# Optimization experiments

Measured on AMD Instinct MI355X. Metric: run time of the kernel, lower is better.

The kernel has to match this reference:

```python
import jax, jax.numpy as jnp
import numpy as np

N_HEADS = 16
DIM = 1024
BS, SLEN = 2, 2048
EPS = 1e-12  # F.normalize eps


def setup_inputs() -> dict:
    key = jax.random.key(0)
    ks = jax.random.split(key, 10)
    d = DIM
    inp = {
        "x": jax.random.normal(ks[0], (BS, SLEN, d), dtype=jnp.float32),
        # causal attention mask, as produced by get_masks(causal=True)
        "mask": jnp.tril(jnp.ones((SLEN, SLEN), dtype=bool))[None].repeat(BS, axis=0),
        "Wq": jax.random.normal(ks[1], (d, d), dtype=jnp.float32) / np.sqrt(d),
        "bq": jax.random.normal(ks[2], (d,), dtype=jnp.float32) * 0.02,
        "Wk": jax.random.normal(ks[3], (d, d), dtype=jnp.float32) / np.sqrt(d),
        "bk": jax.random.normal(ks[4], (d,), dtype=jnp.float32) * 0.02,
        "Wv": jax.random.normal(ks[5], (d, d), dtype=jnp.float32) / np.sqrt(d),
        "bv": jax.random.normal(ks[6], (d,), dtype=jnp.float32) * 0.02,
        "Wo": jax.random.normal(ks[7], (d, d), dtype=jnp.float32) / np.sqrt(d),
        "bo": jax.random.normal(ks[8], (d,), dtype=jnp.float32) * 0.02,
        # learnable scale for normalized (cosine) attention
        "attention_scale": jnp.ones((1,), dtype=jnp.float32) / np.sqrt(d // N_HEADS),
    }
    return inp


def _shape(t, bs, h, dph):
    # (bs, len, dim) -> (bs, h, len, dph)
    return t.reshape(bs, -1, h, dph).transpose(0, 2, 1, 3)


def reference(x, mask, Wq, bq, Wk, bk, Wv, bv, Wo, bo, attention_scale):
    bs, qlen, dim = x.shape
    h = N_HEADS
    dph = dim // h

    q = _shape(x @ Wq + bq, bs, h, dph)  # (bs, h, qlen, dph)
    k = _shape(x @ Wk + bk, bs, h, dph)
    v = _shape(x @ Wv + bv, bs, h, dph)

    # normalized (cosine) attention: L2-normalize q and k, learned scale
    q = q / jnp.maximum(jnp.linalg.norm(q, axis=-1, keepdims=True), EPS)
    k = k / jnp.maximum(jnp.linalg.norm(k, axis=-1, keepdims=True), EPS)
    q = q * attention_scale

    scores = jnp.einsum("bhqd,bhkd->bhqk", q, k)  # (bs, h, qlen, klen)
    scores = jnp.where(mask[:, None, :, :], scores, -jnp.inf)
    weights = jax.nn.softmax(scores, axis=-1)

    ctx = jnp.einsum("bhqk,bhkd->bhqd", weights, v)
    ctx = ctx.transpose(0, 2, 1, 3).reshape(bs, qlen, dim)
    return ctx @ Wo + bo
```

## Files before the change

### kernel.cpp

```cpp
#include <hip/hip_runtime.h>
#include <math.h>

#define NH 16
#define DPH 64
#define SLEN 2048
#define BSZ 2
#define DIM 1024
#define NTOK (BSZ * SLEN)
#define LOG2E 1.44269504088896f

typedef unsigned short ushortT;
typedef __attribute__((ext_vector_type(8))) short short8;
typedef __attribute__((ext_vector_type(4))) short s16x4;
typedef __attribute__((ext_vector_type(4))) float f32x4;

typedef __attribute__((address_space(1))) const unsigned int gu32c;
typedef __attribute__((address_space(3))) unsigned int lu32;

__device__ __forceinline__ void gld16(const void* g, void* l) {
    __builtin_amdgcn_global_load_lds((gu32c*)g, (lu32*)l, 16, 0, 0);
}

__device__ __forceinline__ ushortT f2bf(float f) {
    unsigned int u = __builtin_bit_cast(unsigned int, f);
    u = u + 0x7fffu + ((u >> 16) & 1u);
    return (ushortT)(u >> 16);
}

__device__ __forceinline__ unsigned int cvtpk_bf16(float a, float b) {
    unsigned int r;
    asm("v_cvt_pk_bf16_f32 %0, %1, %2" : "=v"(r) : "v"(a), "v"(b));
    return r;
}

__global__ __launch_bounds__(256) void cvt_all(const float* __restrict__ x,
                                               ushortT* __restrict__ xb,
                                               const float* __restrict__ W0, const float* __restrict__ W1,
                                               const float* __restrict__ W2, const float* __restrict__ W3,
                                               ushortT* __restrict__ T0, ushortT* __restrict__ T1,
                                               ushortT* __restrict__ T2, ushortT* __restrict__ T3) {
    __shared__ float tile[64][65];
    const int tid = threadIdx.x;
    const int bid = blockIdx.x;
    if (bid < 2048) {
        size_t i = (size_t)bid * 256 + tid;
        float4 a = *(const float4*)&x[i * 8];
        float4 b = *(const float4*)&x[i * 8 + 4];
        short8 v;
        v[0] = (short)f2bf(a.x); v[1] = (short)f2bf(a.y);
        v[2] = (short)f2bf(a.z); v[3] = (short)f2bf(a.w);
        v[4] = (short)f2bf(b.x); v[5] = (short)f2bf(b.y);
        v[6] = (short)f2bf(b.z); v[7] = (short)f2bf(b.w);
        *(short8*)&xb[i * 8] = v;
        return;
    }
    const int widx = bid - 2048;
    const int z = widx >> 8, rem = widx & 255;
    const float* W = z == 0 ? W0 : z == 1 ? W1 : z == 2 ? W2 : W3;
    ushortT* T = z == 0 ? T0 : z == 1 ? T1 : z == 2 ? T2 : T3;
    const int kb = (rem >> 4) * 64, nb = (rem & 15) * 64;
#pragma unroll
    for (int it = 0; it < 4; it++) {
        int chunk = it * 256 + tid;
        int r = chunk >> 4, c4 = (chunk & 15) * 4;
        *(float4*)&tile[r][c4] = *(const float4*)&W[(size_t)(kb + r) * DIM + nb + c4];
    }
    __syncthreads();
#pragma unroll
    for (int it = 0; it < 2; it++) {
        int chunk = it * 256 + tid;
        int n = chunk >> 3, k8 = (chunk & 7) * 8;
        short8 o;
#pragma unroll
        for (int j = 0; j < 8; j++) o[j] = (short)f2bf(tile[k8 + j][n]);
        *(short8*)&T[(size_t)(nb + n) * DIM + kb + k8] = o;
    }
}

__global__ __launch_bounds__(512, 2) void gemm_qkv8(const ushortT* __restrict__ A,
                                                    const ushortT* __restrict__ Bt,
                                                    const float* __restrict__ bq,
                                                    const float* __restrict__ bk,
                                                    const float* __restrict__ bv,
                                                    const float* __restrict__ ascale,
                                                    ushortT* __restrict__ Qb,
                                                    ushortT* __restrict__ Kb,
                                                    ushortT* __restrict__ VF) {
    __shared__ __align__(16) ushortT lds[65536];
    const int tid = threadIdx.x;
    const int lane = tid & 63, wid = tid >> 6;
    const int wm = wid >> 2, wn = wid & 3;
    const int lo = lane & 15, hi = lane >> 4;
    const int bid = blockIdx.x;
    const int swz = (bid & 7) * 24 + (bid >> 3);
    const int bx = swz % 12, by = swz / 12;
    const int row0 = by * 256, col0 = bx * 256;
    const int srow2 = tid >> 2, sc = tid & 3;
    f32x4 acc[8][4] = {};
    short8 af[4], bfr[4];

    auto stage = [&](int isA, int buf, int ksh, int kt) {
        const ushortT* g = isA ? A : Bt;
        int r0 = isA ? row0 : col0;
        int base = (isA ? 0 : 32768) + (buf * 2 + ksh) * 8192;
#pragma unroll
        for (int r = 0; r < 2; r++) {
            int rl = r * 128 + srow2;
            int gch = sc ^ ((rl >> 1) & 3);
            gld16(&g[(size_t)(r0 + rl) * DIM + kt * 64 + ksh * 32 + gch * 8],
                  &lds[base + r * 4096 + tid * 8]);
        }
    };
    auto loadA = [&](int buf, int ks, int mh) {
        int base = (buf * 2 + ks) * 8192;
#pragma unroll
        for (int mm = 0; mm < 4; mm++) {
            int row = wm * 128 + (mh * 4 + mm) * 16 + lo;
            af[mm] = *(const short8*)&lds[base + row * 32 + (hi ^ ((row >> 1) & 3)) * 8];
        }
    };
    auto loadB = [&](int buf, int ks) {
        int base = 32768 + (buf * 2 + ks) * 8192;
#pragma unroll
        for (int n = 0; n < 4; n++) {
            int row = wn * 64 + n * 16 + lo;
            bfr[n] = *(const short8*)&lds[base + row * 32 + (hi ^ ((row >> 1) & 3)) * 8];
        }
    };
    auto mfma16 = [&](int mh) {
        __builtin_amdgcn_s_setprio(1);
#pragma unroll
        for (int mm = 0; mm < 4; mm++)
#pragma unroll
            for (int n = 0; n < 4; n++)
                acc[mh * 4 + mm][n] = __builtin_amdgcn_mfma_f32_16x16x32_bf16(
                    af[mm], bfr[n], acc[mh * 4 + mm][n], 0, 0, 0);
        __builtin_amdgcn_s_setprio(0);
    };

    stage(1, 0, 0, 0); stage(0, 0, 0, 0);
    stage(1, 0, 1, 0); stage(0, 0, 1, 0);
    stage(1, 1, 0, 1); stage(0, 1, 0, 1);

#pragma unroll 1
    for (int it = 0; it < 8; ++it) {
        const int o = it * 2 + 1;
        const bool more = (it < 7);
        asm volatile("s_waitcnt vmcnt(8)" ::: "memory");
        asm volatile("s_barrier" ::: "memory");
        loadA(0, 0, 0); loadB(0, 0);
        stage(1, 1, 1, o);
        mfma16(0);
        asm volatile("s_barrier" ::: "memory");
        loadA(0, 0, 1);
        stage(0, 1, 1, o);
        mfma16(1);
        asm volatile("s_waitcnt vmcnt(8)" ::: "memory");
        asm volatile("s_barrier" ::: "memory");
        loadA(0, 1, 0); loadB(0, 1);
        if (more) stage(1, 0, 0, o + 1);
        mfma16(0);
        asm volatile("s_barrier" ::: "memory");
        loadA(0, 1, 1);
        if (more) stage(0, 0, 0, o + 1);
        mfma16(1);
        if (more) { asm volatile("s_waitcnt vmcnt(8)" ::: "memory"); }
        else      { asm volatile("s_waitcnt vmcnt(4)" ::: "memory"); }
        asm volatile("s_barrier" ::: "memory");
        loadA(1, 0, 0); loadB(1, 0);
        if (more) stage(1, 0, 1, o + 1);
        mfma16(0);
        asm volatile("s_barrier" ::: "memory");
        loadA(1, 0, 1);
        if (more) stage(0, 0, 1, o + 1);
        mfma16(1);
        if (more) { asm volatile("s_waitcnt vmcnt(8)" ::: "memory"); }
        else      { asm volatile("s_waitcnt vmcnt(0)" ::: "memory"); }
        asm volatile("s_barrier" ::: "memory");
        loadA(1, 1, 0); loadB(1, 1);
        if (more) stage(1, 1, 0, o + 2);
        mfma16(0);
        asm volatile("s_barrier" ::: "memory");
        loadA(1, 1, 1);
        if (more) stage(0, 1, 0, o + 2);
        mfma16(1);
    }
    __syncthreads();

    const int cg = col0 + wn * 64;
    const int which = cg >> 10;
    const int cwin = cg & 1023;
    const int h = cwin >> 6;
    const int t0g = row0 + wm * 128;
    const int b = t0g >> 11, tok0 = t0g & (SLEN - 1);
    const float* bias = which == 0 ? bq : which == 1 ? bk : bv;

    float bb4[4];
#pragma unroll
    for (int n = 0; n < 4; n++) bb4[n] = bias[cwin + n * 16 + lo];
#pragma unroll
    for (int m = 0; m < 8; m++)
#pragma unroll
        for (int n = 0; n < 4; n++)
#pragma unroll
            for (int r = 0; r < 4; r++) acc[m][n][r] += bb4[n];

    if (which < 2) {
        float asc = (which == 0) ? ascale[0] * LOG2E : 1.0f;
#pragma unroll
        for (int m = 0; m < 8; m++)
#pragma unroll
            for (int r = 0; r < 4; r++) {
                float ss = acc[m][0][r] * acc[m][0][r] + acc[m][1][r] * acc[m][1][r] +
                           acc[m][2][r] * acc[m][2][r] + acc[m][3][r] * acc[m][3][r];
#pragma unroll
                for (int o = 8; o > 0; o >>= 1) ss += __shfl_xor(ss, o);
                float sc2 = asc / fmaxf(sqrtf(ss), 1e-12f);
#pragma unroll
                for (int n = 0; n < 4; n++) acc[m][n][r] *= sc2;
            }
    }

    ushortT* tl = &lds[wid * 8192];
    if (which < 2) {
#pragma unroll
        for (int m = 0; m < 8; m++)
#pragma unroll
            for (int n = 0; n < 4; n++)
#pragma unroll
                for (int r = 0; r < 4; r++) {
                    int row = m * 16 + 4 * hi + r;
                    int c = n * 2 + (lo >> 3);
                    tl[row * 64 + ((c ^ (row & 7)) << 3) + (lo & 7)] = f2bf(acc[m][n][r]);
                }
        ushortT* op = which == 0 ? Qb : Kb;
        const size_t base = ((size_t)(b * NH + h) * SLEN + tok0) * DPH;
#pragma unroll
        for (int j = 0; j < 16; j++) {
            int cid = j * 64 + lane;
            int rowL = cid >> 3, c = cid & 7;
            uint4 v = *(const uint4*)&tl[rowL * 64 + ((c ^ (rowL & 7)) << 3)];
            *(uint4*)&op[base + (size_t)cid * 8] = v;
        }
    } else {
#pragma unroll
        for (int m = 0; m < 8; m++)
#pragma unroll
            for (int n = 0; n < 4; n++)
#pragma unroll
                for (int r = 0; r < 4; r++) {
                    int row = m * 16 + 4 * hi + r;
                    int c = n * 2 + (lo >> 3);
                    tl[row * 64 + ((c ^ ((row >> 3) & 7)) << 3) + (lo & 7)] = f2bf(acc[m][n][r]);
                }
        const int bh = b * NH + h;
        const int kt0 = tok0 >> 6;
#pragma unroll
        for (int i = 0; i < 16; i++) {
            int kk = i >> 3;
            int c = i & 7;
            int jd = c >> 1, ks2 = c & 1;
            int colL = jd * 16 + lo;
            int c2 = colL >> 3;
            short8 v;
#pragma unroll
            for (int e = 0; e < 8; e++) {
                int rowL = kk * 64 + ks2 * 32 + 8 * hi + e;
                v[e] = (short)tl[rowL * 64 + ((c2 ^ ((rowL >> 3) & 7)) << 3) + (colL & 7)];
            }
            *(short8*)&VF[((size_t)bh * 32 + kt0 + kk) * 4096 + (size_t)(c * 64 + lane) * 8] = v;
        }
    }
}

__global__ __launch_bounds__(512, 2) void gemm_oproj(const ushortT* __restrict__ A,
                                                     const ushortT* __restrict__ Bt,
                                                     const float* __restrict__ bias,
                                                     float* __restrict__ outF) {
    __shared__ __align__(16) ushortT lds[32768];
    const int tid = threadIdx.x;
    const int lane = tid & 63, wid = tid >> 6;
    const int wm = wid >> 2, wn = wid & 3;
    const int lo = lane & 15, hi = lane >> 4;
    const int bid = blockIdx.x;
    const int swz = (bid & 7) * 32 + (bid >> 3);
    const int bx = swz & 7, by = swz >> 3;
    const int row0 = by * 128, col0 = bx * 128;
    const int srow = tid >> 2, sc = tid & 3;
    f32x4 acc[4][2] = {};
    short8 afO[2], bfO[2];

    auto stage = [&](int isA, int buf, int ksh, int kt) {
        const ushortT* g = isA ? A : Bt;
        int r0 = isA ? row0 : col0;
        int base = (isA ? 0 : 16384) + (buf * 2 + ksh) * 4096;
        int gch = sc ^ ((srow >> 1) & 3);
        gld16(&g[(size_t)(r0 + srow) * DIM + kt * 64 + ksh * 32 + gch * 8],
              &lds[base + tid * 8]);
    };
    auto loadAO = [&](int buf, int ks, int mh) {
        int base = (buf * 2 + ks) * 4096;
#pragma unroll
        for (int mm = 0; mm < 2; mm++) {
            int row = wm * 64 + (mh * 2 + mm) * 16 + lo;
            afO[mm] = *(const short8*)&lds[base + row * 32 + (hi ^ ((row >> 1) & 3)) * 8];
        }
    };
    auto loadBO = [&](int buf, int ks) {
        int base = 16384 + (buf * 2 + ks) * 4096;
#pragma unroll
        for (int n = 0; n < 2; n++) {
            int row = wn * 32 + n * 16 + lo;
            bfO[n] = *(const short8*)&lds[base + row * 32 + (hi ^ ((row >> 1) & 3)) * 8];
        }
    };
    auto mfma4 = [&](int mh) {
        __builtin_amdgcn_s_setprio(1);
#pragma unroll
        for (int mm = 0; mm < 2; mm++)
#pragma unroll
            for (int n = 0; n < 2; n++)
                acc[mh * 2 + mm][n] = __builtin_amdgcn_mfma_f32_16x16x32_bf16(
                    afO[mm], bfO[n], acc[mh * 2 + mm][n], 0, 0, 0);
        __builtin_amdgcn_s_setprio(0);
    };

    stage(1, 0, 0, 0); stage(0, 0, 0, 0);
    stage(1, 0, 1, 0); stage(0, 0, 1, 0);
    stage(1, 1, 0, 1); stage(0, 1, 0, 1);

#pragma unroll 1
    for (int it = 0; it < 8; ++it) {
        const int o = it * 2 + 1;
        const bool more = (it < 7);
        asm volatile("s_waitcnt vmcnt(4)" ::: "memory");
        asm volatile("s_barrier" ::: "memory");
        loadAO(0, 0, 0); loadBO(0, 0);
        stage(1, 1, 1, o);
        mfma4(0);
        asm volatile("s_barrier" ::: "memory");
        loadAO(0, 0, 1);
        stage(0, 1, 1, o);
        mfma4(1);
        asm volatile("s_waitcnt vmcnt(4)" ::: "memory");
        asm volatile("s_barrier" ::: "memory");
        loadAO(0, 1, 0); loadBO(0, 1);
        if (more) stage(1, 0, 0, o + 1);
        mfma4(0);
        asm volatile("s_barrier" ::: "memory");
        loadAO(0, 1, 1);
        if (more) stage(0, 0, 0, o + 1);
        mfma4(1);
        if (more) { asm volatile("s_waitcnt vmcnt(4)" ::: "memory"); }
        else      { asm volatile("s_waitcnt vmcnt(2)" ::: "memory"); }
        asm volatile("s_barrier" ::: "memory");
        loadAO(1, 0, 0); loadBO(1, 0);
        if (more) stage(1, 0, 1, o + 1);
        mfma4(0);
        asm volatile("s_barrier" ::: "memory");
        loadAO(1, 0, 1);
        if (more) stage(0, 0, 1, o + 1);
        mfma4(1);
        if (more) { asm volatile("s_waitcnt vmcnt(4)" ::: "memory"); }
        else      { asm volatile("s_waitcnt vmcnt(0)" ::: "memory"); }
        asm volatile("s_barrier" ::: "memory");
        loadAO(1, 1, 0); loadBO(1, 1);
        if (more) stage(1, 1, 0, o + 2);
        mfma4(0);
        asm volatile("s_barrier" ::: "memory");
        loadAO(1, 1, 1);
        if (more) stage(0, 1, 0, o + 2);
        mfma4(1);
    }
    __syncthreads();

    float bb[2];
#pragma unroll
    for (int n = 0; n < 2; n++) bb[n] = bias[col0 + wn * 32 + n * 16 + lo];
#pragma unroll
    for (int m = 0; m < 4; m++)
#pragma unroll
        for (int n = 0; n < 2; n++)
#pragma unroll
            for (int r = 0; r < 4; r++) acc[m][n][r] += bb[n];

    float* tl = (float*)&lds[wid * 4096];
#pragma unroll
    for (int m = 0; m < 4; m++)
#pragma unroll
        for (int n = 0; n < 2; n++)
#pragma unroll
            for (int r = 0; r < 4; r++) {
                int row = m * 16 + hi * 4 + r;
                int col = n * 16 + lo;
                int cc = col >> 2;
                tl[row * 32 + ((cc ^ (row & 7)) << 2) + (col & 3)] = acc[m][n][r];
            }
#pragma unroll
    for (int j = 0; j < 8; j++) {
        int cid = j * 64 + lane;
        int rowR = cid >> 3, cc = cid & 7;
        f32x4 v = *(const f32x4*)&tl[rowR * 32 + ((cc ^ (rowR & 7)) << 2)];
        int rg = row0 + wm * 64 + rowR;
        int cgl = col0 + wn * 32 + cc * 4;
        *(f32x4*)&outF[(size_t)rg * DIM + cgl] = v;
    }
}

__global__ __launch_bounds__(512, 4) void attn(const ushortT* __restrict__ Q,
                                               const ushortT* __restrict__ K,
                                               const ushortT* __restrict__ VF,
                                               const float* __restrict__ scale,
                                               ushortT* __restrict__ ctx) {
    __shared__ __align__(16) ushortT Ks[2][64 * 64];
    __shared__ __align__(16) ushortT Ps[8 * 16 * 64];
    const int tid = threadIdx.x, lane = tid & 63, wid = tid >> 6;
    const int wg = wid & 3, sg = wid >> 2;
    const int bh = blockIdx.x, p = blockIdx.y;
    const int qt = sg ? p : 31 - p;
    const int kbmax = 31 - p;
    const size_t hb = (size_t)bh * SLEN * DPH;
    const int lo = lane & 15, hi = lane >> 4;
    const float mshift = fabsf(scale[0]) * LOG2E;

    short8 aq[2];
    {
        const int qrow = qt * 64 + wg * 16 + lo;
#pragma unroll
        for (int ks = 0; ks < 2; ks++)
            aq[ks] = *(const short8*)&Q[hb + (size_t)qrow * DPH + ks * 32 + 8 * hi];
    }

    const int srow = tid >> 3, sslot = tid & 7;
    const int sldsoff = srow * 64 + ((sslot ^ (srow & 7)) << 3);
    uint4 kr = *(const uint4*)&K[hb + (size_t)srow * DPH + sslot * 8];
    *(uint4*)&Ks[0][sldsoff] = kr;
    __syncthreads();

    f32x4 accd[4] = {};
    float lp = 0.f;

    for (int kb = 0; kb <= kbmax; kb++) {
        const int cur = kb & 1;
        if (kb < kbmax)
            kr = *(const uint4*)&K[hb + (size_t)((kb + 1) * 64 + srow) * DPH + sslot * 8];

        if (kb <= qt) {
            short8 bv[8];
            const ushortT* vt = &VF[(((size_t)bh * 32 + kb) * 512 + lane) * 8];
#pragma unroll
            for (int c = 0; c < 8; c++) bv[c] = *(const short8*)&vt[(size_t)c * 512];

            f32x4 sf[4] = {};
            __builtin_amdgcn_s_setprio(1);
#pragma unroll
            for (int ks = 0; ks < 2; ks++)
#pragma unroll
                for (int j = 0; j < 4; j++) {
                    int row = j * 16 + lo;
                    short8 bk = *(const short8*)&Ks[cur][row * 64 + (((ks * 4 + hi) ^ (row & 7)) << 3)];
                    sf[j] = __builtin_amdgcn_mfma_f32_16x16x32_bf16(bk, aq[ks], sf[j], 0, 0, 0);
                }
            __builtin_amdgcn_s_setprio(0);

            if (kb == qt) {
#pragma unroll
                for (int j = 0; j < 4; j++)
#pragma unroll
                    for (int r = 0; r < 4; r++)
                        if (j * 16 + 4 * hi + r > wg * 16 + lo) sf[j][r] = -INFINITY;
            }

#pragma unroll
            for (int j = 0; j < 4; j++) {
                float pv0 = __builtin_amdgcn_exp2f(sf[j][0] - mshift);
                float pv1 = __builtin_amdgcn_exp2f(sf[j][1] - mshift);
                float pv2 = __builtin_amdgcn_exp2f(sf[j][2] - mshift);
                float pv3 = __builtin_amdgcn_exp2f(sf[j][3] - mshift);
                lp += (pv0 + pv1) + (pv2 + pv3);
                uint2 pk;
                pk.x = cvtpk_bf16(pv0, pv1);
                pk.y = cvtpk_bf16(pv2, pv3);
                int slot = (4 * j + hi) ^ (2 * (lo & 7));
                *(uint2*)&Ps[wid * 1024 + lo * 64 + slot * 4] = pk;
            }

            __builtin_amdgcn_s_setprio(1);
#pragma unroll
            for (int ks = 0; ks < 2; ks++) {
                int slot0 = (8 * ks + 2 * hi) ^ (2 * (lo & 7));
                short8 ap = *(const short8*)&Ps[wid * 1024 + lo * 64 + slot0 * 4];
#pragma unroll
                for (int jd = 0; jd < 4; jd++)
                    accd[jd] = __builtin_amdgcn_mfma_f32_16x16x32_bf16(ap, bv[jd * 2 + ks], accd[jd], 0, 0, 0);
            }
            __builtin_amdgcn_s_setprio(0);
        }

        if (kb < kbmax) *(uint4*)&Ks[cur ^ 1][sldsoff] = kr;
        __syncthreads();
    }

    lp += __shfl_xor(lp, 16);
    lp += __shfl_xor(lp, 32);

    const int b = bh >> 4, h = bh & 15;
#pragma unroll
    for (int r = 0; r < 4; r++) {
        float lr = __shfl(lp, (lane & 48) | (4 * hi + r));
        float inv = 1.0f / lr;
        int t = qt * 64 + wg * 16 + 4 * hi + r;
#pragma unroll
        for (int jd = 0; jd < 4; jd++) {
            int d = jd * 16 + lo;
            ctx[(size_t)(b * SLEN + t) * DIM + h * 64 + d] = f2bf(accd[jd][r] * inv);
        }
    }
}

extern "C" void kernel_launch(void* const* d_in, const int* in_sizes, int n_in,
                              void* d_out, int out_size, void* d_ws,
                              size_t ws_size, hipStream_t stream) {
    const float* x = (const float*)d_in[0];
    const float* Wq = (const float*)d_in[2];
    const float* bq = (const float*)d_in[3];
    const float* Wk = (const float*)d_in[4];
    const float* bk = (const float*)d_in[5];
    const float* Wv = (const float*)d_in[6];
    const float* bv = (const float*)d_in[7];
    const float* Wo = (const float*)d_in[8];
    const float* bo = (const float*)d_in[9];
    const float* ascale = (const float*)d_in[10];
    float* outF = (float*)d_out;

    unsigned char* ws = (unsigned char*)d_ws;
    const size_t MB = 1u << 20;
    ushortT* xb = (ushortT*)(ws);
    ushortT* Wqkvt = (ushortT*)(ws + 8 * MB);
    ushortT* Wot = (ushortT*)(ws + 14 * MB);
    ushortT* Qb = (ushortT*)(ws + 16 * MB);
    ushortT* Kb = (ushortT*)(ws + 24 * MB);
    ushortT* VFb = (ushortT*)(ws + 32 * MB);
    ushortT* ctxb = (ushortT*)(ws + 40 * MB);

    cvt_all<<<3072, 256, 0, stream>>>(x, xb, Wq, Wk, Wv, Wo, Wqkvt,
                                      Wqkvt + (size_t)1024 * 1024,
                                      Wqkvt + (size_t)2048 * 1024, Wot);

    gemm_qkv8<<<dim3(192), 512, 0, stream>>>(xb, Wqkvt, bq, bk, bv, ascale, Qb, Kb, VFb);

    attn<<<dim3(32, 16), 512, 0, stream>>>(Qb, Kb, VFb, ascale, ctxb);

    gemm_oproj<<<dim3(256), 512, 0, stream>>>(ctxb, Wot, bo, outF);
}
```

Baseline: 94.25 us.

## Simplify QKV GEMM pipeline to double-buffer and process two K tiles per attention barrier

The QKV projection GEMM drops its triple-stage interleaved schedule, with half-tile MFMA groups and a barrier between each, for a plain double-buffered loop. Each half-K step now loads all eight A fragments and issues 32 MFMAs between barriers. The attention kernel stages two 64-row K tiles per round in a doubled LDS buffer, halving the number of __syncthreads per key block. This cuts barrier and scheduling overhead but raises register pressure (af[8]) and LDS use, which may reduce overlap or occupancy.

```diff
diff --git a/kernel.cpp b/kernel.cpp
--- a/kernel.cpp
+++ b/kernel.cpp
@@ -11,7 +11,6 @@
 
 typedef unsigned short ushortT;
 typedef __attribute__((ext_vector_type(8))) short short8;
-typedef __attribute__((ext_vector_type(4))) short s16x4;
 typedef __attribute__((ext_vector_type(4))) float f32x4;
 
 typedef __attribute__((address_space(1))) const unsigned int gu32c;
@@ -97,7 +96,7 @@
     const int row0 = by * 256, col0 = bx * 256;
     const int srow2 = tid >> 2, sc = tid & 3;
     f32x4 acc[8][4] = {};
-    short8 af[4], bfr[4];
+    short8 af[8], bfr[4];
 
     auto stage = [&](int isA, int buf, int ksh, int kt) {
         const ushortT* g = isA ? A : Bt;
@@ -111,11 +110,11 @@
                   &lds[base + r * 4096 + tid * 8]);
         }
     };
-    auto loadA = [&](int buf, int ks, int mh) {
+    auto loadA8 = [&](int buf, int ks) {
         int base = (buf * 2 + ks) * 8192;
 #pragma unroll
-        for (int mm = 0; mm < 4; mm++) {
-            int row = wm * 128 + (mh * 4 + mm) * 16 + lo;
+        for (int mm = 0; mm < 8; mm++) {
+            int row = wm * 128 + mm * 16 + lo;
             af[mm] = *(const short8*)&lds[base + row * 32 + (hi ^ ((row >> 1) & 3)) * 8];
         }
     };
@@ -127,63 +126,35 @@
             bfr[n] = *(const short8*)&lds[base + row * 32 + (hi ^ ((row >> 1) & 3)) * 8];
         }
     };
-    auto mfma16 = [&](int mh) {
+    auto mfma32 = [&]() {
         __builtin_amdgcn_s_setprio(1);
 #pragma unroll
-        for (int mm = 0; mm < 4; mm++)
+        for (int mm = 0; mm < 8; mm++)
 #pragma unroll
             for (int n = 0; n < 4; n++)
-                acc[mh * 4 + mm][n] = __builtin_amdgcn_mfma_f32_16x16x32_bf16(
-                    af[mm], bfr[n], acc[mh * 4 + mm][n], 0, 0, 0);
+                acc[mm][n] = __builtin_amdgcn_mfma_f32_16x16x32_bf16(
+                    af[mm], bfr[n], acc[mm][n], 0, 0, 0);
         __builtin_amdgcn_s_setprio(0);
     };
 
-    stage(1, 0, 0, 0); stage(0, 0, 0, 0);
-    stage(1, 0, 1, 0); stage(0, 0, 1, 0);
-    stage(1, 1, 0, 1); stage(0, 1, 0, 1);
+    stage(0, 0, 0, 0); stage(1, 0, 0, 0);
+    stage(0, 0, 1, 0); stage(1, 0, 1, 0);
 
 #pragma unroll 1
-    for (int it = 0; it < 8; ++it) {
-        const int o = it * 2 + 1;
-        const bool more = (it < 7);
-        asm volatile("s_waitcnt vmcnt(8)" ::: "memory");
-        asm volatile("s_barrier" ::: "memory");
-        loadA(0, 0, 0); loadB(0, 0);
-        stage(1, 1, 1, o);
-        mfma16(0);
-        asm volatile("s_barrier" ::: "memory");
-        loadA(0, 0, 1);
-        stage(0, 1, 1, o);
-        mfma16(1);
-        asm volatile("s_waitcnt vmcnt(8)" ::: "memory");
-        asm volatile("s_barrier" ::: "memory");
-        loadA(0, 1, 0); loadB(0, 1);
-        if (more) stage(1, 0, 0, o + 1);
-        mfma16(0);
-        asm volatile("s_barrier" ::: "memory");
-        loadA(0, 1, 1);
-        if (more) stage(0, 0, 0, o + 1);
-        mfma16(1);
-        if (more) { asm volatile("s_waitcnt vmcnt(8)" ::: "memory"); }
-        else      { asm volatile("s_waitcnt vmcnt(4)" ::: "memory"); }
-        asm volatile("s_barrier" ::: "memory");
-        loadA(1, 0, 0); loadB(1, 0);
-        if (more) stage(1, 0, 1, o + 1);
-        mfma16(0);
-        asm volatile("s_barrier" ::: "memory");
-        loadA(1, 0, 1);
-        if (more) stage(0, 0, 1, o + 1);
-        mfma16(1);
-        if (more) { asm volatile("s_waitcnt vmcnt(8)" ::: "memory"); }
+    for (int t = 0; t < 16; ++t) {
+        const int cur = t & 1, nxt = cur ^ 1;
+        const bool more = (t < 15);
+        asm volatile("s_waitcnt vmcnt(4)" ::: "memory");
+        asm volatile("s_barrier" ::: "memory");
+        loadA8(cur, 0); loadB(cur, 0);
+        if (more) { stage(0, nxt, 0, t + 1); stage(1, nxt, 0, t + 1); }
+        mfma32();
+        if (more) { asm volatile("s_waitcnt vmcnt(4)" ::: "memory"); }
         else      { asm volatile("s_waitcnt vmcnt(0)" ::: "memory"); }
         asm volatile("s_barrier" ::: "memory");
-        loadA(1, 1, 0); loadB(1, 1);
-        if (more) stage(1, 1, 0, o + 2);
-        mfma16(0);
-        asm volatile("s_barrier" ::: "memory");
-        loadA(1, 1, 1);
-        if (more) stage(0, 1, 0, o + 2);
-        mfma16(1);
+        loadA8(cur, 1); loadB(cur, 1);
+        if (more) { stage(0, nxt, 1, t + 1); stage(1, nxt, 1, t + 1); }
+        mfma32();
     }
     __syncthreads();
 
@@ -412,7 +383,7 @@
                                                const ushortT* __restrict__ VF,
                                                const float* __restrict__ scale,
                                                ushortT* __restrict__ ctx) {
-    __shared__ __align__(16) ushortT Ks[2][64 * 64];
+    __shared__ __align__(16) ushortT Ks[2][2][64 * 64];
     __shared__ __align__(16) ushortT Ps[8 * 16 * 64];
     const int tid = threadIdx.x, lane = tid & 63, wid = tid >> 6;
     const int wg = wid & 3, sg = wid >> 2;
@@ -433,71 +404,83 @@
 
     const int srow = tid >> 3, sslot = tid & 7;
     const int sldsoff = srow * 64 + ((sslot ^ (srow & 7)) << 3);
-    uint4 kr = *(const uint4*)&K[hb + (size_t)srow * DPH + sslot * 8];
-    *(uint4*)&Ks[0][sldsoff] = kr;
+    {
+        uint4 k0 = *(const uint4*)&K[hb + (size_t)srow * DPH + sslot * 8];
+        uint4 k1 = *(const uint4*)&K[hb + (size_t)(64 + srow) * DPH + sslot * 8];
+        *(uint4*)&Ks[0][0][sldsoff] = k0;
+        *(uint4*)&Ks[0][1][sldsoff] = k1;
+    }
     __syncthreads();
 
     f32x4 accd[4] = {};
     float lp = 0.f;
 
-    for (int kb = 0; kb <= kbmax; kb++) {
-        const int cur = kb & 1;
-        if (kb < kbmax)
-            kr = *(const uint4*)&K[hb + (size_t)((kb + 1) * 64 + srow) * DPH + sslot * 8];
-
-        if (kb <= qt) {
-            short8 bv[8];
-            const ushortT* vt = &VF[(((size_t)bh * 32 + kb) * 512 + lane) * 8];
-#pragma unroll
-            for (int c = 0; c < 8; c++) bv[c] = *(const short8*)&vt[(size_t)c * 512];
-
-            f32x4 sf[4] = {};
-            __builtin_amdgcn_s_setprio(1);
-#pragma unroll
-            for (int ks = 0; ks < 2; ks++)
+    for (int rd = 0; rd * 2 <= kbmax; ++rd) {
+        const int cur = rd & 1;
+        const int tn0 = 2 * rd + 2, tn1 = 2 * rd + 3;
+        const bool h0 = tn0 <= kbmax, h1 = tn1 <= kbmax;
+        uint4 n0, n1;
+        if (h0) n0 = *(const uint4*)&K[hb + (size_t)(tn0 * 64 + srow) * DPH + sslot * 8];
+        if (h1) n1 = *(const uint4*)&K[hb + (size_t)(tn1 * 64 + srow) * DPH + sslot * 8];
+
+#pragma unroll
+        for (int sub = 0; sub < 2; ++sub) {
+            const int kb = 2 * rd + sub;
+            if (kb <= qt) {
+                short8 bv[8];
+                const ushortT* vt = &VF[(((size_t)bh * 32 + kb) * 512 + lane) * 8];
+#pragma unroll
+                for (int c = 0; c < 8; c++) bv[c] = *(const short8*)&vt[(size_t)c * 512];
+
+                f32x4 sf[4] = {};
+                __builtin_amdgcn_s_setprio(1);
+#pragma unroll
+                for (int ks = 0; ks < 2; ks++)
+#pragma unroll
+                    for (int j = 0; j < 4; j++) {
+                        int row = j * 16 + lo;
+                        short8 bk = *(const short8*)&Ks[cur][sub][row * 64 + (((ks * 4 + hi) ^ (row & 7)) << 3)];
+                        sf[j] = __builtin_amdgcn_mfma_f32_16x16x32_bf16(bk, aq[ks], sf[j], 0, 0, 0);
+                    }
+                __builtin_amdgcn_s_setprio(0);
+
+                if (kb == qt) {
+#pragma unroll
+                    for (int j = 0; j < 4; j++)
+#pragma unroll
+                        for (int r = 0; r < 4; r++)
+                            if (j * 16 + 4 * hi + r > wg * 16 + lo) sf[j][r] = -INFINITY;
+                }
+
 #pragma unroll
                 for (int j = 0; j < 4; j++) {
-                    int row = j * 16 + lo;
-                    short8 bk = *(const short8*)&Ks[cur][row * 64 + (((ks * 4 + hi) ^ (row & 7)) << 3)];
-                    sf[j] = __builtin_amdgcn_mfma_f32_16x16x32_bf16(bk, aq[ks], sf[j], 0, 0, 0);
+                    float pv0 = __builtin_amdgcn_exp2f(sf[j][0] - mshift);
+                    float pv1 = __builtin_amdgcn_exp2f(sf[j][1] - mshift);
+                    float pv2 = __builtin_amdgcn_exp2f(sf[j][2] - mshift);
+                    float pv3 = __builtin_amdgcn_exp2f(sf[j][3] - mshift);
+                    lp += (pv0 + pv1) + (pv2 + pv3);
+                    uint2 pk;
+                    pk.x = cvtpk_bf16(pv0, pv1);
+                    pk.y = cvtpk_bf16(pv2, pv3);
+                    int slot = (4 * j + hi) ^ (2 * (lo & 7));
+                    *(uint2*)&Ps[wid * 1024 + lo * 64 + slot * 4] = pk;
                 }
-            __builtin_amdgcn_s_setprio(0);
-
-            if (kb == qt) {
-#pragma unroll
-                for (int j = 0; j < 4; j++)
-#pragma unroll
-                    for (int r = 0; r < 4; r++)
-                        if (j * 16 + 4 * hi + r > wg * 16 + lo) sf[j][r] = -INFINITY;
+
+                __builtin_amdgcn_s_setprio(1);
+#pragma unroll
+                for (int ks = 0; ks < 2; ks++) {
+                    int slot0 = (8 * ks + 2 * hi) ^ (2 * (lo & 7));
+                    short8 ap = *(const short8*)&Ps[wid * 1024 + lo * 64 + slot0 * 4];
+#pragma unroll
+                    for (int jd = 0; jd < 4; jd++)
+                        accd[jd] = __builtin_amdgcn_mfma_f32_16x16x32_bf16(ap, bv[jd * 2 + ks], accd[jd], 0, 0, 0);
+                }
+                __builtin_amdgcn_s_setprio(0);
             }
-
-#pragma unroll
-            for (int j = 0; j < 4; j++) {
-                float pv0 = __builtin_amdgcn_exp2f(sf[j][0] - mshift);
-                float pv1 = __builtin_amdgcn_exp2f(sf[j][1] - mshift);
-                float pv2 = __builtin_amdgcn_exp2f(sf[j][2] - mshift);
-                float pv3 = __builtin_amdgcn_exp2f(sf[j][3] - mshift);
-                lp += (pv0 + pv1) + (pv2 + pv3);
-                uint2 pk;
-                pk.x = cvtpk_bf16(pv0, pv1);
-                pk.y = cvtpk_bf16(pv2, pv3);
-                int slot = (4 * j + hi) ^ (2 * (lo & 7));
-                *(uint2*)&Ps[wid * 1024 + lo * 64 + slot * 4] = pk;
-            }
-
-            __builtin_amdgcn_s_setprio(1);
-#pragma unroll
-            for (int ks = 0; ks < 2; ks++) {
-                int slot0 = (8 * ks + 2 * hi) ^ (2 * (lo & 7));
-                short8 ap = *(const short8*)&Ps[wid * 1024 + lo * 64 + slot0 * 4];
-#pragma unroll
-                for (int jd = 0; jd < 4; jd++)
-                    accd[jd] = __builtin_amdgcn_mfma_f32_16x16x32_bf16(ap, bv[jd * 2 + ks], accd[jd], 0, 0, 0);
-            }
-            __builtin_amdgcn_s_setprio(0);
-        }
-
-        if (kb < kbmax) *(uint4*)&Ks[cur ^ 1][sldsoff] = kr;
+        }
+
+        if (h0) *(uint4*)&Ks[cur ^ 1][0][sldsoff] = n0;
+        if (h1) *(uint4*)&Ks[cur ^ 1][1][sldsoff] = n1;
         __syncthreads();
     }
 
```

After: 95.64 us. About the same (+1.5%).
